# Optimization experiments

Measured on AMD Instinct MI355X. Metric: run time of the kernel, lower is better.

The kernel has to match this reference:

```python
import jax, jax.numpy as jnp
import numpy as np

N = 50000      # nodes
E = 800000     # edges (before self-loops)
DIN = 2        # dim_input
DEMB = 128     # dim_embedding
H = 8          # n_heads
DV = 16        # dim_values (H*DV == DEMB)
DH = 512       # dim_hidden
L = 2          # n_att_layers
K = 10         # APPNP steps
ALPHA = 0.1
EPS = 1e-5     # BatchNorm eps
NEG_SLOPE = 0.2  # GAT leaky_relu slope


def setup_inputs() -> dict:
    key = jax.random.key(0)
    ks = jax.random.split(key, 16)
    s = 0.05
    inp = {}
    inp["x"] = jax.random.normal(ks[0], (N, DIN), jnp.float32)
    inp["J"] = jax.random.uniform(ks[1], (N, 1), jnp.float32)
    inp["edge_index"] = jax.random.randint(ks[2], (2, E), 0, N, jnp.int32)
    # Lin1: Linear(dim_input+1, dim_embedding)
    inp["lin0_w"] = jax.random.normal(ks[3], (DIN + 1, DEMB), jnp.float32) * s
    inp["lin0_b"] = jnp.zeros((DEMB,), jnp.float32)
    # Per attention layer (stacked over L):
    inp["gat_w"]   = jax.random.normal(ks[4], (L, DEMB, H * DV), jnp.float32) * s
    inp["att_src"] = jax.random.normal(ks[5], (L, H, DV), jnp.float32) * s
    inp["att_dst"] = jax.random.normal(ks[6], (L, H, DV), jnp.float32) * s
    inp["lin1_w"]  = jax.random.normal(ks[7], (L, DV, DEMB), jnp.float32) * s
    inp["bn1_g"]   = jnp.ones((L, DEMB), jnp.float32)
    inp["bn1_b"]   = jnp.zeros((L, DEMB), jnp.float32)
    inp["lin2_w"]  = jax.random.normal(ks[8], (L, DEMB, DH), jnp.float32) * s
    inp["lin2_b"]  = jnp.zeros((L, DH), jnp.float32)
    inp["lin3_w"]  = jax.random.normal(ks[9], (L, DH, DEMB), jnp.float32) * s
    inp["lin3_b"]  = jnp.zeros((L, DEMB), jnp.float32)
    inp["bn2_g"]   = jnp.ones((L, DEMB), jnp.float32)
    inp["bn2_b"]   = jnp.zeros((L, DEMB), jnp.float32)
    return inp


def _bn(z, g, b):
    # BatchNorm1d over nodes, training-mode batch statistics (biased var)
    mu = z.mean(0)
    var = jnp.mean((z - mu) ** 2, axis=0)
    return g * (z - mu) * jax.lax.rsqrt(var + EPS) + b


def reference(x, J, edge_index, lin0_w, lin0_b, gat_w, att_src, att_dst,
              lin1_w, bn1_g, bn1_b, lin2_w, lin2_b, lin3_w, lin3_b,
              bn2_g, bn2_b):
    # add self-loops (PyG GATConv and APPNP defaults)
    loop = jnp.arange(N, dtype=edge_index.dtype)
    src = jnp.concatenate([edge_index[0], loop])  # message source j
    dst = jnp.concatenate([edge_index[1], loop])  # message target i

    h = jnp.concatenate([x, J], axis=1) @ lin0_w + lin0_b  # [N, DEMB]

    for l in range(L):
        # ---- GATConv ----
        xl = (h @ gat_w[l]).reshape(N, H, DV)                # [N,H,DV]
        a_s = (xl * att_src[l]).sum(-1)                      # [N,H]
        a_d = (xl * att_dst[l]).sum(-1)                      # [N,H]
        e = jax.nn.leaky_relu(a_s[src] + a_d[dst], NEG_SLOPE)  # [E',H]
        e = e - jax.ops.segment_max(e, dst, num_segments=N)[dst]
        ee = jnp.exp(e)
        alpha = ee / jax.ops.segment_sum(ee, dst, num_segments=N)[dst]
        msg = xl[src] * alpha[:, :, None]                    # [E',H,DV]
        gat_out = jax.ops.segment_sum(msg, dst, num_segments=N)  # [N,H,DV]
        # lin1 per head then sum over heads
        hsum = jnp.einsum('nhc,cd->nd', gat_out, lin1_w[l])  # [N,DEMB]
        h1 = _bn(h + hsum, bn1_g[l], bn1_b[l])
        h2 = jax.nn.relu(h1 @ lin2_w[l] + lin2_b[l]) @ lin3_w[l] + lin3_b[l]
        h = _bn(h2 + h1, bn2_g[l], bn2_b[l])

    # ---- APPNP: K steps of (1-a)*Ahat h + a*h0, Ahat = D^-1/2 (A+I) D^-1/2 ----
    deg = jax.ops.segment_sum(jnp.ones_like(dst, jnp.float32), dst, num_segments=N)
    dinv = jax.lax.rsqrt(jnp.maximum(deg, 1.0))  # self-loops guarantee deg>=1
    norm = (dinv[src] * dinv[dst])[:, None]      # [E',1]
    h0 = h

    def step(hk, _):
        agg = jax.ops.segment_sum(norm * hk[src], dst, num_segments=N)
        return (1.0 - ALPHA) * agg + ALPHA * h0, None

    h, _ = jax.lax.scan(step, h, None, length=K)
    return jnp.concatenate([h, J], axis=1)  # [N, DEMB+1]
```

## Files before the change

kernel.cpp:

```cpp
#include <hip/hip_runtime.h>

#define NN 50000
#define NP 50048
#define NMT64 782
#define NE 800000
#define EP (NE + NN)
#define DEMB 128
#define DHID 512
#define NB_SCAN 196

typedef unsigned short ushort_t;
typedef __attribute__((ext_vector_type(8))) short short8_t;
typedef __attribute__((ext_vector_type(4))) float float4_t;

__device__ __forceinline__ float bf2f(ushort_t u) {
    return __uint_as_float(((unsigned int)u) << 16);
}
__device__ __forceinline__ ushort_t f2bf(float f) {
    unsigned int x = __float_as_uint(f);
    x += 0x7fffu + ((x >> 16) & 1u);
    return (ushort_t)(x >> 16);
}
__device__ __forceinline__ float lo16(unsigned int w) { return __uint_as_float(w << 16); }
__device__ __forceinline__ float hi16(unsigned int w) { return __uint_as_float(w & 0xffff0000u); }
__device__ __forceinline__ unsigned int pack2(float a, float b) {
    return (unsigned int)f2bf(a) | ((unsigned int)f2bf(b) << 16);
}
__device__ __forceinline__ void gl_lds16(const ushort_t* g, ushort_t* l) {
    __builtin_amdgcn_global_load_lds(
        (const __attribute__((address_space(1))) void*)g,
        (__attribute__((address_space(3))) void*)l, 16, 0, 0);
}
static inline int cdiv(int a, int b) { return (a + b - 1) / b; }

__global__ void k_detect(const unsigned int* __restrict__ Jw, int* __restrict__ flag) {
    if (threadIdx.x != 0 || blockIdx.x != 0) return;
    int votes = 0;
    for (int i = 0; i < 8; ++i) {
        unsigned int w = Jw[i];
        unsigned int ex = (w >> 23) & 0xFFu;
        if ((w >> 31) == 0u && ex >= 100u && ex <= 126u) votes++;
    }
    *flag = (votes >= 6) ? 1 : 0;
}

struct CvtArgs {
    const void* src[16];
    float* dst[16];
    int n[16];
};
__global__ void k_cvt_all(CvtArgs a, const int* __restrict__ flag) {
    int which = blockIdx.y;
    int i = blockIdx.x * 256 + threadIdx.x;
    if (i >= a.n[which]) return;
    float v;
    if (*flag) v = ((const float*)a.src[which])[i];
    else       v = bf2f(((const ushort_t*)a.src[which])[i]);
    a.dst[which][i] = v;
}

struct TrArgs {
    const float* src[6];
    ushort_t* dst[6];
    int K[6];
    int Nc[6];
    int perm[6];
};
__global__ void k_tr_all(TrArgs a) {
    int which = blockIdx.y;
    int idx = blockIdx.x * 256 + threadIdx.x;
    int K = a.K[which], Nc = a.Nc[which];
    if (idx >= K * Nc) return;
    int k = idx / Nc, n = idx - k * Nc;
    int kd = k;
    if (a.perm[which]) {
        int kk = k & 63;
        kd = (k & ~63) | ((kk & 32) + 2 * (kk & 15) + ((kk >> 4) & 1));
    }
    a.dst[which][n * K + kd] = f2bf(a.src[which][idx]);
}

__global__ void k_deg(const int* __restrict__ ei, int* __restrict__ deg) {
    int e = blockIdx.x * 256 + threadIdx.x;
    if (e >= EP) return;
    int d = (e < NE) ? ei[NE + e] : (e - NE);
    atomicAdd(&deg[d], 1);
}

__global__ void k_part(const int* __restrict__ deg, int* __restrict__ part) {
    __shared__ int sm[256];
    int i = blockIdx.x * 256 + threadIdx.x;
    int v = (i < NN) ? deg[i] : 0;
    sm[threadIdx.x] = v;
    __syncthreads();
    for (int off = 128; off > 0; off >>= 1) {
        if (threadIdx.x < off) sm[threadIdx.x] += sm[threadIdx.x + off];
        __syncthreads();
    }
    if (threadIdx.x == 0) part[blockIdx.x] = sm[0];
}

__global__ void k_scan2(const int* __restrict__ part, int* __restrict__ poff,
                        int* __restrict__ rowp) {
    __shared__ int sm[256];
    int t = threadIdx.x;
    int v = (t < NB_SCAN) ? part[t] : 0;
    sm[t] = v;
    __syncthreads();
    int incl = v;
    for (int off = 1; off < 256; off <<= 1) {
        int u = (t >= off) ? sm[t - off] : 0;
        __syncthreads();
        incl += u;
        sm[t] = incl;
        __syncthreads();
    }
    if (t < NB_SCAN) poff[t] = incl - v;
    if (t == 255) rowp[NN] = sm[255];
}

__global__ void k_rowp(const int* __restrict__ deg, const int* __restrict__ poff,
                       int* __restrict__ rowp, float* __restrict__ dinv,
                       int* __restrict__ fill) {
    __shared__ int sm[256];
    int i = blockIdx.x * 256 + threadIdx.x;
    int t = threadIdx.x;
    int v = (i < NN) ? deg[i] : 0;
    sm[t] = v;
    __syncthreads();
    int incl = v;
    for (int off = 1; off < 256; off <<= 1) {
        int u = (t >= off) ? sm[t - off] : 0;
        __syncthreads();
        incl += u;
        sm[t] = incl;
        __syncthreads();
    }
    if (i < NN) {
        int rp = poff[blockIdx.x] + incl - v;
        rowp[i] = rp;
        fill[i] = rp;
        dinv[i] = rsqrtf(fmaxf((float)v, 1.0f));
    }
}

__global__ void k_fill(const int* __restrict__ ei, int* __restrict__ fillpos,
                       ushort_t* __restrict__ col) {
    int e = blockIdx.x * 256 + threadIdx.x;
    if (e >= EP) return;
    int s, d;
    if (e < NE) { s = ei[e]; d = ei[NE + e]; } else { s = d = e - NE; }
    int pos = atomicAdd(&fillpos[d], 1);
    col[pos] = (ushort_t)s;
}

__global__ void k_lin0(const float* __restrict__ x, const float* __restrict__ J,
                       const float* __restrict__ w, const float* __restrict__ b,
                       ushort_t* __restrict__ hB) {
    int idx = blockIdx.x * 256 + threadIdx.x;
    if (idx >= NN * DEMB) return;
    int n = idx >> 7, d = idx & 127;
    float v = x[n * 2] * w[d] + x[n * 2 + 1] * w[DEMB + d] + J[n] * w[2 * DEMB + d] + b[d];
    hB[idx] = f2bf(v);
}

__global__ void k_att(const unsigned int* __restrict__ xlB, const float* __restrict__ asrc,
                      const float* __restrict__ adst, float* __restrict__ a_s,
                      float* __restrict__ a_d) {
    int idx = blockIdx.x * 256 + threadIdx.x;
    if (idx >= NN * 8) return;
    int n = idx >> 3, hh = idx & 7;
    const unsigned int* row = xlB + (size_t)n * 64 + hh * 8;
    float s = 0.f, d = 0.f;
#pragma unroll
    for (int c = 0; c < 8; ++c) {
        unsigned int w = row[c];
        float v0 = lo16(w), v1 = hi16(w);
        s += v0 * asrc[hh * 16 + 2 * c] + v1 * asrc[hh * 16 + 2 * c + 1];
        d += v0 * adst[hh * 16 + 2 * c] + v1 * adst[hh * 16 + 2 * c + 1];
    }
    a_s[idx] = s;
    a_d[idx] = d;
}

__global__ __launch_bounds__(256) void k_z1s(const ushort_t* __restrict__ hB,
                                             const float* __restrict__ g,
                                             const float* __restrict__ w1,
                                             float* __restrict__ stats) {
    int d = threadIdx.x & 127;
    int rstart = blockIdx.x * 2 + (threadIdx.x >> 7);
    int stride = gridDim.x * 2;
    float s1 = 0.f, s2 = 0.f;
    for (int r = rstart; r < NN; r += stride) {
        const float* gr = g + r * 16;
        float s = bf2f(hB[(size_t)r * DEMB + d]);
#pragma unroll
        for (int c = 0; c < 16; ++c) s += gr[c] * w1[c * DEMB + d];
        s1 += s;
        s2 += s * s;
    }
    __shared__ float b1[256], b2[256];
    b1[threadIdx.x] = s1;
    b2[threadIdx.x] = s2;
    __syncthreads();
    if (threadIdx.x < 128) {
        atomicAdd(&stats[threadIdx.x], b1[threadIdx.x] + b1[threadIdx.x + 128]);
        atomicAdd(&stats[128 + threadIdx.x], b2[threadIdx.x] + b2[threadIdx.x + 128]);
    }
}

__global__ void k_bnapply1(const ushort_t* __restrict__ hB, const float* __restrict__ g,
                           const float* __restrict__ w1, const float* __restrict__ stats,
                           const float* __restrict__ gam, const float* __restrict__ bet,
                           ushort_t* __restrict__ outB) {
    int idx = blockIdx.x * 256 + threadIdx.x;
    if (idx >= NN * DEMB) return;
    int n = idx >> 7, d = idx & 127;
    float s = bf2f(hB[idx]);
    const float* gr = g + n * 16;
#pragma unroll
    for (int c = 0; c < 16; ++c) s += gr[c] * w1[c * DEMB + d];
    const float invN = 1.0f / (float)NN;
    float mu = stats[d] * invN;
    float var = stats[128 + d] * invN - mu * mu;
    float rs = rsqrtf(fmaxf(var, 0.f) + 1e-5f);
    float v = gam[d] * (s - mu) * rs + bet[d];
    outB[idx] = f2bf(v);
}

__global__ void k_bnapply(const ushort_t* __restrict__ zB, const float* __restrict__ stats,
                          const float* __restrict__ gam, const float* __restrict__ bet,
                          ushort_t* __restrict__ outB) {
    int idx = blockIdx.x * 256 + threadIdx.x;
    if (idx >= NN * DEMB) return;
    int d = idx & 127;
    const float invN = 1.0f / (float)NN;
    float mu = stats[d] * invN;
    float var = stats[128 + d] * invN - mu * mu;
    float rs = rsqrtf(fmaxf(var, 0.f) + 1e-5f);
    float v = gam[d] * (bf2f(zB[idx]) - mu) * rs + bet[d];
    outB[idx] = f2bf(v);
}

__global__ void k_bnapply_fin(const unsigned int* __restrict__ zB, const float* __restrict__ stats,
                              const float* __restrict__ gam, const float* __restrict__ bet,
                              const float* __restrict__ dinv,
                              unsigned int* __restrict__ hs, unsigned int* __restrict__ h0p) {
    int idx = blockIdx.x * 256 + threadIdx.x;
    if (idx >= NN * 64) return;
    int n = idx >> 6, d0 = (idx & 63) * 2;
    const float invN = 1.0f / (float)NN;
    unsigned int zw = zB[idx];
    float z0 = lo16(zw), z1 = hi16(zw);
    float mu0 = stats[d0] * invN, mu1 = stats[d0 + 1] * invN;
    float v0 = stats[128 + d0] * invN - mu0 * mu0;
    float v1 = stats[128 + d0 + 1] * invN - mu1 * mu1;
    float rs0 = rsqrtf(fmaxf(v0, 0.f) + 1e-5f);
    float rs1 = rsqrtf(fmaxf(v1, 0.f) + 1e-5f);
    float a = gam[d0] * (z0 - mu0) * rs0 + bet[d0];
    float b = gam[d0 + 1] * (z1 - mu1) * rs1 + bet[d0 + 1];
    float di = dinv[n];
    hs[idx] = pack2(di * a, di * b);
    h0p[idx] = pack2(a, b);
}

__global__ __launch_bounds__(256) void k_gat(const int* __restrict__ rowp,
                                             const ushort_t* __restrict__ col,
                                             const float* __restrict__ a_s, const float* __restrict__ a_d,
                                             const unsigned int* __restrict__ xlB, float* __restrict__ g) {
    int wid = (blockIdx.x * 256 + threadIdx.x) >> 6;
    int lane = threadIdx.x & 63;
    if (wid >= NN) return;
    int p0 = rowp[wid], p1 = rowp[wid + 1];
    int hh = lane >> 3;
    float ad2 = a_d[wid * 8 + hh];
    float acc0 = 0.f, acc1 = 0.f, s = 0.f;
    int p = p0;
    while (p < p1) {
        int cnt = p1 - p;
        if (cnt > 64) cnt = 64;
        int pl = p + lane;
        int jv = (int)col[pl < p1 ? pl : (p1 - 1)];
        int i = 0;
        for (; i + 8 <= cnt; i += 8) {
            int j0 = __shfl(jv, i),     j1 = __shfl(jv, i + 1);
            int j2 = __shfl(jv, i + 2), j3 = __shfl(jv, i + 3);
            int j4 = __shfl(jv, i + 4), j5 = __shfl(jv, i + 5);
            int j6 = __shfl(jv, i + 6), j7 = __shfl(jv, i + 7);
            float e0 = a_s[j0 * 8 + hh] + ad2, e1 = a_s[j1 * 8 + hh] + ad2;
            float e2 = a_s[j2 * 8 + hh] + ad2, e3 = a_s[j3 * 8 + hh] + ad2;
            float e4 = a_s[j4 * 8 + hh] + ad2, e5 = a_s[j5 * 8 + hh] + ad2;
            float e6 = a_s[j6 * 8 + hh] + ad2, e7 = a_s[j7 * 8 + hh] + ad2;
            unsigned int w0 = xlB[j0 * 64 + lane], w1 = xlB[j1 * 64 + lane];
            unsigned int w2 = xlB[j2 * 64 + lane], w3 = xlB[j3 * 64 + lane];
            unsigned int w4 = xlB[j4 * 64 + lane], w5 = xlB[j5 * 64 + lane];
            unsigned int w6 = xlB[j6 * 64 + lane], w7 = xlB[j7 * 64 + lane];
            e0 = e0 > 0.f ? e0 : 0.2f * e0;  e1 = e1 > 0.f ? e1 : 0.2f * e1;
            e2 = e2 > 0.f ? e2 : 0.2f * e2;  e3 = e3 > 0.f ? e3 : 0.2f * e3;
            e4 = e4 > 0.f ? e4 : 0.2f * e4;  e5 = e5 > 0.f ? e5 : 0.2f * e5;
            e6 = e6 > 0.f ? e6 : 0.2f * e6;  e7 = e7 > 0.f ? e7 : 0.2f * e7;
            float al0 = __expf(e0), al1 = __expf(e1), al2 = __expf(e2), al3 = __expf(e3);
            float al4 = __expf(e4), al5 = __expf(e5), al6 = __expf(e6), al7 = __expf(e7);
            s += al0 + al1 + al2 + al3 + al4 + al5 + al6 + al7;
            acc0 += al0 * lo16(w0) + al1 * lo16(w1) + al2 * lo16(w2) + al3 * lo16(w3) +
                    al4 * lo16(w4) + al5 * lo16(w5) + al6 * lo16(w6) + al7 * lo16(w7);
            acc1 += al0 * hi16(w0) + al1 * hi16(w1) + al2 * hi16(w2) + al3 * hi16(w3) +
                    al4 * hi16(w4) + al5 * hi16(w5) + al6 * hi16(w6) + al7 * hi16(w7);
        }
        for (; i < cnt; ++i) {
            int j = __shfl(jv, i);
            float e = a_s[j * 8 + hh] + ad2;
            e = e > 0.f ? e : 0.2f * e;
            float al = __expf(e);
            unsigned int w = xlB[j * 64 + lane];
            s += al;
            acc0 += al * lo16(w);
            acc1 += al * hi16(w);
        }
        p += cnt;
    }
    float inv = 1.f / s;
    acc0 *= inv;
    acc1 *= inv;
    acc0 += __shfl_xor(acc0, 8);  acc1 += __shfl_xor(acc1, 8);
    acc0 += __shfl_xor(acc0, 16); acc1 += __shfl_xor(acc1, 16);
    acc0 += __shfl_xor(acc0, 32); acc1 += __shfl_xor(acc1, 32);
    if (lane < 8) ((float2*)g)[wid * 8 + lane] = make_float2(acc0, acc1);
}

__global__ __launch_bounds__(256) void k_appnp(const int* __restrict__ rowp,
                                               const ushort_t* __restrict__ col,
                                               const float* __restrict__ dinv,
                                               const unsigned int* __restrict__ hs,
                                               const unsigned int* __restrict__ h0p,
                                               unsigned int* __restrict__ hs_out,
                                               const float* __restrict__ Jf,
                                               const int* __restrict__ flag,
                                               void* __restrict__ out, int writeOut) {
    int wid = (blockIdx.x * 256 + threadIdx.x) >> 6;
    int lane = threadIdx.x & 63;
    if (wid >= NN) return;
    int p0 = rowp[wid], p1 = rowp[wid + 1];
    float di = dinv[wid];
    unsigned int hw = h0p[(size_t)wid * 64 + lane];
    float a0 = 0.f, a1 = 0.f;
    int p = p0;
    while (p < p1) {
        int cnt = p1 - p;
        if (cnt > 64) cnt = 64;
        int pl = p + lane;
        int jv = (int)col[pl < p1 ? pl : (p1 - 1)];
        int i = 0;
        for (; i + 8 <= cnt; i += 8) {
            int j0 = __shfl(jv, i),     j1 = __shfl(jv, i + 1);
            int j2 = __shfl(jv, i + 2), j3 = __shfl(jv, i + 3);
            int j4 = __shfl(jv, i + 4), j5 = __shfl(jv, i + 5);
            int j6 = __shfl(jv, i + 6), j7 = __shfl(jv, i + 7);
            unsigned int w0 = hs[j0 * 64 + lane], w1 = hs[j1 * 64 + lane];
            unsigned int w2 = hs[j2 * 64 + lane], w3 = hs[j3 * 64 + lane];
            unsigned int w4 = hs[j4 * 64 + lane], w5 = hs[j5 * 64 + lane];
            unsigned int w6 = hs[j6 * 64 + lane], w7 = hs[j7 * 64 + lane];
            a0 += lo16(w0) + lo16(w1) + lo16(w2) + lo16(w3) +
                  lo16(w4) + lo16(w5) + lo16(w6) + lo16(w7);
            a1 += hi16(w0) + hi16(w1) + hi16(w2) + hi16(w3) +
                  hi16(w4) + hi16(w5) + hi16(w6) + hi16(w7);
        }
        for (; i < cnt; ++i) {
            int j = __shfl(jv, i);
            unsigned int w = hs[j * 64 + lane];
            a0 += lo16(w);
            a1 += hi16(w);
        }
        p += cnt;
    }
    float n0 = 0.9f * di * a0 + 0.1f * lo16(hw);
    float n1 = 0.9f * di * a1 + 0.1f * hi16(hw);
    if (!writeOut) {
        hs_out[(size_t)wid * 64 + lane] = pack2(di * n0, di * n1);
    } else {
        size_t base = (size_t)wid * 129;
        if (*flag) {
            float* o = (float*)out;
            o[base + 2 * lane] = n0;
            o[base + 2 * lane + 1] = n1;
            if (lane == 0) o[base + 128] = Jf[wid];
        } else {
            ushort_t* o = (ushort_t*)out;
            o[base + 2 * lane] = f2bf(n0);
            o[base + 2 * lane + 1] = f2bf(n1);
            if (lane == 0) o[base + 128] = f2bf(Jf[wid]);
        }
    }
}

template <int MODE>
__global__ __launch_bounds__(256) void k_gemm64(const ushort_t* __restrict__ A,
                                                const ushort_t* __restrict__ Bt,
                                                int M, int K, int Nc,
                                                const float* __restrict__ bias,
                                                const ushort_t* __restrict__ res,
                                                ushort_t* __restrict__ outB,
                                                float* __restrict__ stats) {
    __shared__ __align__(16) ushort_t lsA[2][64 * 32];
    __shared__ __align__(16) ushort_t lsB[2][128 * 32];
    int t = threadIdx.x;
    int m0 = blockIdx.x * 64;
    int n0 = blockIdx.y * 128;
    int w = t >> 6, lane = t & 63;
    int row16 = lane & 15, quad = lane >> 4;
    int nbase = w * 32;
    float4_t acc[8];
#pragma unroll
    for (int i = 0; i < 8; ++i) acc[i] = (float4_t){0.f, 0.f, 0.f, 0.f};
    int lrow = lane >> 2;
    int lcol = (lane & 3) * 8;
    const ushort_t* gA  = A  + (size_t)(m0 + w * 16 + lrow) * K + lcol;
    const ushort_t* gB0 = Bt + (size_t)(n0 + w * 32 + lrow) * K + lcol;
    const ushort_t* gB1 = Bt + (size_t)(n0 + w * 32 + 16 + lrow) * K + lcol;
    ushort_t* dA  = &lsA[0][0] + (w * 16) * 32;
    ushort_t* dB0 = &lsB[0][0] + (w * 32) * 32;
    ushort_t* dB1 = &lsB[0][0] + (w * 32 + 16) * 32;
    const int bufStrideA = 64 * 32, bufStrideB = 128 * 32;
    const int nK = K >> 5;
    gl_lds16(gA, dA);
    gl_lds16(gB0, dB0);
    gl_lds16(gB1, dB1);
    for (int kb = 0; kb < nK; ++kb) {
        __syncthreads();
        int nb = kb + 1;
        if (nb < nK) {
            int b = nb & 1;
            int k0 = nb << 5;
            gl_lds16(gA + k0, dA + b * bufStrideA);
            gl_lds16(gB0 + k0, dB0 + b * bufStrideB);
            gl_lds16(gB1 + k0, dB1 + b * bufStrideB);
        }
        const ushort_t* la = &lsA[kb & 1][0];
        const ushort_t* lb = &lsB[kb & 1][0];
        short8_t afr[4], bfr[2];
#pragma unroll
        for (int i = 0; i < 4; ++i)
            afr[i] = *(const short8_t*)(la + (i * 16 + row16) * 32 + quad * 8);
#pragma unroll
        for (int i = 0; i < 2; ++i)
            bfr[i] = *(const short8_t*)(lb + (nbase + i * 16 + row16) * 32 + quad * 8);
#pragma unroll
        for (int mt = 0; mt < 4; ++mt)
#pragma unroll
            for (int nt = 0; nt < 2; ++nt)
                acc[mt * 2 + nt] = __builtin_amdgcn_mfma_f32_16x16x32_bf16(
                    afr[mt], bfr[nt], acc[mt * 2 + nt], 0, 0, 0);
    }
#pragma unroll
    for (int mt = 0; mt < 4; ++mt) {
#pragma unroll
        for (int nt = 0; nt < 2; ++nt) {
            int cc = n0 + nbase + nt * 16 + row16;
#pragma unroll
            for (int r = 0; r < 4; ++r) {
                int rr = m0 + mt * 16 + quad * 4 + r;
                if (rr < M) {
                    outB[(size_t)rr * Nc + cc] = f2bf(acc[mt * 2 + nt][r]);
                }
            }
        }
    }
}

__global__ __launch_bounds__(256, 3) void k_ffn(const ushort_t* __restrict__ A,
                                                const ushort_t* __restrict__ W2t,
                                                const ushort_t* __restrict__ W3t,
                                                const float* __restrict__ b2,
                                                const float* __restrict__ b3,
                                                const ushort_t* __restrict__ res,
                                                ushort_t* __restrict__ outB,
                                                float* __restrict__ stats) {
    __shared__ __align__(16) ushort_t sW2[4 * 64 * 32];
    __shared__ __align__(16) ushort_t sW3[2 * 128 * 32];
    __shared__ __align__(16) ushort_t sAH[4 * 2048];
    int t = threadIdx.x;
    int w = t >> 6, lane = t & 63;
    int wm = w >> 1, wn = w & 1;
    int m0 = blockIdx.x * 64;
    int row16 = lane & 15, quad = lane >> 4;
    int sw = (row16 >> 2) & 3;
    int srow = lane >> 2;
    int klin = lane & 3;

#pragma unroll
    for (int i = 0; i < 4; ++i) {
        int row = i * 16 + srow;
        int kc = klin ^ ((row >> 2) & 3);
        gl_lds16(A + (size_t)(m0 + row) * 128 + w * 32 + kc * 8,
                 sAH + w * 2048 + i * 512);
        gl_lds16(W2t + (size_t)row * 128 + w * 32 + kc * 8,
                 sW2 + w * 2048 + i * 512);
        int f = w * 4 + i;
        int ks = f >> 3;
        int n3 = (f & 7) * 16 + srow;
        int kc3 = klin ^ ((n3 >> 2) & 3);
        gl_lds16(W3t + (size_t)n3 * 512 + ks * 32 + kc3 * 8,
                 sW3 + f * 512);
    }
    __syncthreads();

    short8_t afrA[2][4];
#pragma unroll
    for (int mt = 0; mt < 2; ++mt)
#pragma unroll
        for (int kb = 0; kb < 4; ++kb)
            afrA[mt][kb] = *(const short8_t*)(sAH + kb * 2048 +
                                              (wm * 32 + mt * 16 + row16) * 32 + (quad ^ sw) * 8);
    __syncthreads();

    char* Hb = (char*)sAH;
    float* s1 = (float*)(Hb + 8192);
    float* s2 = s1 + 128;
    if (t < 128) { s1[t] = 0.f; s2[t] = 0.f; }

    float4_t accz[2][4];
#pragma unroll
    for (int mt = 0; mt < 2; ++mt)
#pragma unroll
        for (int nt = 0; nt < 4; ++nt) accz[mt][nt] = (float4_t){0.f, 0.f, 0.f, 0.f};

    for (int c = 0; c < 8; ++c) {
        float b20 = b2[c * 64 + wn * 32 + row16];
        float b21 = b2[c * 64 + wn * 32 + 16 + row16];
        float4_t acch[2][2];
#pragma unroll
        for (int mt = 0; mt < 2; ++mt)
#pragma unroll
            for (int nt = 0; nt < 2; ++nt) acch[mt][nt] = (float4_t){0.f, 0.f, 0.f, 0.f};
#pragma unroll
        for (int kb = 0; kb < 4; ++kb) {
            short8_t b0 = *(const short8_t*)(sW2 + kb * 2048 +
                                             (wn * 32 + row16) * 32 + (quad ^ sw) * 8);
            short8_t b1 = *(const short8_t*)(sW2 + kb * 2048 +
                                             (wn * 32 + 16 + row16) * 32 + (quad ^ sw) * 8);
            acch[0][0] = __builtin_amdgcn_mfma_f32_16x16x32_bf16(afrA[0][kb], b0, acch[0][0], 0, 0, 0);
            acch[0][1] = __builtin_amdgcn_mfma_f32_16x16x32_bf16(afrA[0][kb], b1, acch[0][1], 0, 0, 0);
            acch[1][0] = __builtin_amdgcn_mfma_f32_16x16x32_bf16(afrA[1][kb], b0, acch[1][0], 0, 0, 0);
            acch[1][1] = __builtin_amdgcn_mfma_f32_16x16x32_bf16(afrA[1][kb], b1, acch[1][1], 0, 0, 0);
        }
#pragma unroll
        for (int mt = 0; mt < 2; ++mt) {
#pragma unroll
            for (int r = 0; r < 4; ++r) {
                int row = wm * 32 + mt * 16 + quad * 4 + r;
                int d = wn * 16 + row16;
                int byteOff = row * 128 + ((((d >> 2) ^ (row & 7))) << 4) + (d & 3) * 4;
                float v0 = acch[mt][0][r] + b20; v0 = v0 > 0.f ? v0 : 0.f;
                float v1 = acch[mt][1][r] + b21; v1 = v1 > 0.f ? v1 : 0.f;
                *(unsigned int*)(Hb + byteOff) = pack2(v0, v1);
            }
        }
        __syncthreads();
        if (c < 7) {
#pragma unroll
            for (int i = 0; i < 4; ++i) {
                int n = i * 16 + srow;
                int kc = klin ^ ((n >> 2) & 3);
                gl_lds16(W2t + (size_t)((c + 1) * 64 + n) * 128 + w * 32 + kc * 8,
                         sW2 + w * 2048 + i * 512);
            }
        }
#pragma unroll
        for (int ks = 0; ks < 2; ++ks) {
            short8_t afrH[2];
#pragma unroll
            for (int mt = 0; mt < 2; ++mt)
                afrH[mt] = *(const short8_t*)(Hb + (wm * 32 + mt * 16 + row16) * 128 +
                                              (((ks * 4 + quad) ^ (row16 & 7)) << 4));
#pragma unroll
            for (int nt = 0; nt < 4; ++nt) {
                short8_t bfr = *(const short8_t*)(sW3 + ks * 4096 +
                                                  (wn * 64 + nt * 16 + row16) * 32 + (quad ^ sw) * 8);
                accz[0][nt] = __builtin_amdgcn_mfma_f32_16x16x32_bf16(afrH[0], bfr, accz[0][nt], 0, 0, 0);
                accz[1][nt] = __builtin_amdgcn_mfma_f32_16x16x32_bf16(afrH[1], bfr, accz[1][nt], 0, 0, 0);
            }
        }
        __syncthreads();
        if (c < 7) {
#pragma unroll
            for (int i = 0; i < 4; ++i) {
                int f = w * 4 + i;
                int ks = f >> 3;
                int n = (f & 7) * 16 + srow;
                int kc = klin ^ ((n >> 2) & 3);
                gl_lds16(W3t + (size_t)n * 512 + (c + 1) * 64 + ks * 32 + kc * 8,
                         sW3 + f * 512);
            }
        }
    }

#pragma unroll
    for (int mt = 0; mt < 2; ++mt) {
#pragma unroll
        for (int nt = 0; nt < 4; ++nt) {
            int cc = wn * 64 + nt * 16 + row16;
            float bv = b3[cc];
            float ls = 0.f, lq = 0.f;
#pragma unroll
            for (int r = 0; r < 4; ++r) {
                int rr = m0 + wm * 32 + mt * 16 + quad * 4 + r;
                if (rr < NN) {
                    float v = accz[mt][nt][r] + bv + bf2f(res[(size_t)rr * 128 + cc]);
                    outB[(size_t)rr * 128 + cc] = f2bf(v);
                    ls += v;
                    lq += v * v;
                }
            }
            atomicAdd(&s1[cc], ls);
            atomicAdd(&s2[cc], lq);
        }
    }
    __syncthreads();
    if (t < 128) {
        atomicAdd(&stats[t], s1[t]);
        atomicAdd(&stats[128 + t], s2[t]);
    }
}

extern "C" void kernel_launch(void* const* d_in, const int* in_sizes, int n_in,
                              void* d_out, int out_size, void* d_ws, size_t ws_size,
                              hipStream_t stream) {
    const int* ei = (const int*)d_in[2];

    char* p = (char*)d_ws;
    auto alloc = [&](size_t bytes) {
        void* r = (void*)p;
        p += (bytes + 255) & ~(size_t)255;
        return r;
    };
    ushort_t* hB    = (ushort_t*)alloc((size_t)NP * DEMB * 2);
    ushort_t* h1B   = (ushort_t*)alloc((size_t)NP * DEMB * 2);
    ushort_t* xlB   = (ushort_t*)alloc((size_t)NN * DEMB * 2);
    unsigned int* hsA  = (unsigned int*)alloc((size_t)NN * 64 * 4);
    unsigned int* hsB_ = (unsigned int*)alloc((size_t)NN * 64 * 4);
    unsigned int* h0p  = (unsigned int*)alloc((size_t)NN * 64 * 4);
    float*    asv   = (float*)alloc((size_t)NN * 8 * 4);
    float*    adv   = (float*)alloc((size_t)NN * 8 * 4);
    float*    gv    = (float*)alloc((size_t)NN * 16 * 4);
    float*    dinvv = (float*)alloc((size_t)NN * 4);
    float*    stats = (float*)alloc(4 * 256 * 4);
    int*      deg   = (int*)alloc((size_t)NN * 4);
    int*      rowp  = (int*)alloc((size_t)(NN + 1) * 4);
    int*      fill  = (int*)alloc((size_t)NN * 4);
    ushort_t* colv  = (ushort_t*)alloc((size_t)EP * 2);
    int*      part  = (int*)alloc(NB_SCAN * 4);
    int*      poff  = (int*)alloc(NB_SCAN * 4);
    int*      flag  = (int*)alloc(256);
    ushort_t* wtg   = (ushort_t*)alloc((size_t)2 * 128 * 128 * 2);
    ushort_t* wt2   = (ushort_t*)alloc((size_t)2 * 512 * 128 * 2);
    ushort_t* wt3   = (ushort_t*)alloc((size_t)2 * 128 * 512 * 2);
    float* xf   = (float*)alloc((size_t)NN * 2 * 4);
    float* Jf   = (float*)alloc((size_t)NN * 4);
    float* l0wF = (float*)alloc(384 * 4);
    float* l0bF = (float*)alloc(128 * 4);
    float* gwF  = (float*)alloc(32768 * 4);
    float* asF  = (float*)alloc(256 * 4);
    float* adF  = (float*)alloc(256 * 4);
    float* w1F  = (float*)alloc(4096 * 4);
    float* b1gF = (float*)alloc(256 * 4);
    float* b1bF = (float*)alloc(256 * 4);
    float* w2F  = (float*)alloc(131072 * 4);
    float* b2F  = (float*)alloc(1024 * 4);
    float* w3F  = (float*)alloc(131072 * 4);
    float* b3F  = (float*)alloc(256 * 4);
    float* b2gF = (float*)alloc(256 * 4);
    float* b2bF = (float*)alloc(256 * 4);

    k_detect<<<1, 64, 0, stream>>>((const unsigned int*)d_in[1], flag);
    CvtArgs ca;
    {
        const int srcIdx[16] = {0, 1, 3, 4, 5, 6, 7, 8, 9, 10, 11, 12, 13, 14, 15, 16};
        float* dsts[16] = {xf, Jf, l0wF, l0bF, gwF, asF, adF, w1F, b1gF, b1bF,
                           w2F, b2F, w3F, b3F, b2gF, b2bF};
        const int ns[16] = {NN * 2, NN, 384, 128, 32768, 256, 256, 4096, 256, 256,
                            131072, 1024, 131072, 256, 256, 256};
        for (int i = 0; i < 16; ++i) { ca.src[i] = d_in[srcIdx[i]]; ca.dst[i] = dsts[i]; ca.n[i] = ns[i]; }
    }
    k_cvt_all<<<dim3(cdiv(131072, 256), 16), 256, 0, stream>>>(ca, flag);

    hipMemsetAsync(deg, 0, (size_t)NN * 4, stream);
    hipMemsetAsync(stats, 0, 4 * 256 * 4, stream);
    k_deg<<<cdiv(EP, 256), 256, 0, stream>>>(ei, deg);
    k_part<<<NB_SCAN, 256, 0, stream>>>(deg, part);
    k_scan2<<<1, 256, 0, stream>>>(part, poff, rowp);
    k_rowp<<<NB_SCAN, 256, 0, stream>>>(deg, poff, rowp, dinvv, fill);
    k_fill<<<cdiv(EP, 256), 256, 0, stream>>>(ei, fill, colv);

    TrArgs ta;
    {
        const float* srcs[6] = {gwF, gwF + 16384, w2F, w2F + 65536, w3F, w3F + 65536};
        ushort_t* dsts[6] = {wtg, wtg + 16384, wt2, wt2 + 65536, wt3, wt3 + 65536};
        const int Ks[6] = {128, 128, 128, 128, 512, 512};
        const int Ncs[6] = {128, 128, 512, 512, 128, 128};
        const int perms[6] = {0, 0, 0, 0, 1, 1};
        for (int i = 0; i < 6; ++i) {
            ta.src[i] = srcs[i]; ta.dst[i] = dsts[i]; ta.K[i] = Ks[i]; ta.Nc[i] = Ncs[i];
            ta.perm[i] = perms[i];
        }
    }
    k_tr_all<<<dim3(cdiv(65536, 256), 6), 256, 0, stream>>>(ta);

    k_lin0<<<cdiv(NN * DEMB, 256), 256, 0, stream>>>(xf, Jf, l0wF, l0bF, hB);

    for (int l = 0; l < 2; ++l) {
        float* st1 = stats + (l * 2 + 0) * 256;
        float* st2 = stats + (l * 2 + 1) * 256;
        ushort_t* zB = xlB;
        k_gemm64<3><<<dim3(NMT64, 1), 256, 0, stream>>>(hB, wtg + l * 16384, NN, 128, 128,
                                                        nullptr, nullptr, xlB, nullptr);
        k_att<<<cdiv(NN * 8, 256), 256, 0, stream>>>((const unsigned int*)xlB, asF + l * 128,
                                                     adF + l * 128, asv, adv);
        k_gat<<<cdiv(NN * 64, 256), 256, 0, stream>>>(rowp, colv, asv, adv,
                                                      (const unsigned int*)xlB, gv);
        k_z1s<<<512, 256, 0, stream>>>(hB, gv, w1F + l * 2048, st1);
        k_bnapply1<<<cdiv(NN * DEMB, 256), 256, 0, stream>>>(hB, gv, w1F + l * 2048, st1,
                                                             b1gF + l * 128, b1bF + l * 128,
                                                             h1B);
        k_ffn<<<NMT64, 256, 0, stream>>>(h1B, wt2 + l * 65536, wt3 + l * 65536,
                                         b2F + l * 512, b3F + l * 128, h1B, zB, st2);
        if (l == 0) {
            k_bnapply<<<cdiv(NN * DEMB, 256), 256, 0, stream>>>(zB, st2, b2gF, b2bF, hB);
        } else {
            k_bnapply_fin<<<cdiv(NN * 64, 256), 256, 0, stream>>>((const unsigned int*)zB, st2,
                                                                  b2gF + 128, b2bF + 128,
                                                                  dinvv, hsA, h0p);
        }
    }

    unsigned int* pin = hsA;
    unsigned int* pout = hsB_;
    for (int k = 0; k < 10; ++k) {
        int last = (k == 9) ? 1 : 0;
        k_appnp<<<cdiv(NN * 64, 256), 256, 0, stream>>>(rowp, colv, dinvv, pin, h0p, pout,
                                                        Jf, flag, d_out, last);
        unsigned int* tmp = pout;
        pout = pin;
        pin = tmp;
    }
}
```

Measured before the change: 875.2 us.

## Split APPNP features into column slabs and shrink FFN row tile to 32

The APPNP state is stored as four feature slabs of 32 bf16 features each, laid out node-major within a slab. Each propagation block handles one slab for four nodes, with four edges gathered in parallel per wave. The aim is to keep the gathered working set small enough to stay cache-resident and so cut scattered HBM traffic over the ten propagation steps. Separately, the FFN kernel uses 32-row tiles with each wave owning a column strip, which removes the W3 k-permutation in favour of a shuffle-based pack and allows higher occupancy, at the cost of twice as many blocks and more weight reloads.

```diff
diff --git a/kernel.cpp b/kernel.cpp
--- a/kernel.cpp
+++ b/kernel.cpp
@@ -3,6 +3,7 @@
 #define NN 50000
 #define NP 50048
 #define NMT64 782
+#define NMT32 1563
 #define NE 800000
 #define EP (NE + NN)
 #define DEMB 128
@@ -72,12 +73,7 @@
     int K = a.K[which], Nc = a.Nc[which];
     if (idx >= K * Nc) return;
     int k = idx / Nc, n = idx - k * Nc;
-    int kd = k;
-    if (a.perm[which]) {
-        int kk = k & 63;
-        kd = (k & ~63) | ((kk & 32) + 2 * (kk & 15) + ((kk >> 4) & 1));
-    }
-    a.dst[which][n * K + kd] = f2bf(a.src[which][idx]);
+    a.dst[which][n * K + k] = f2bf(a.src[which][idx]);
 }
 
 __global__ void k_deg(const int* __restrict__ ei, int* __restrict__ deg) {
@@ -248,7 +244,8 @@
                               unsigned int* __restrict__ hs, unsigned int* __restrict__ h0p) {
     int idx = blockIdx.x * 256 + threadIdx.x;
     if (idx >= NN * 64) return;
-    int n = idx >> 6, d0 = (idx & 63) * 2;
+    int n = idx >> 6, j = idx & 63;
+    int d0 = j * 2;
     const float invN = 1.0f / (float)NN;
     unsigned int zw = zB[idx];
     float z0 = lo16(zw), z1 = hi16(zw);
@@ -260,8 +257,10 @@
     float a = gam[d0] * (z0 - mu0) * rs0 + bet[d0];
     float b = gam[d0 + 1] * (z1 - mu1) * rs1 + bet[d0 + 1];
     float di = dinv[n];
-    hs[idx] = pack2(di * a, di * b);
-    h0p[idx] = pack2(a, b);
+    int q = j >> 4, dd = j & 15;
+    size_t o = (size_t)q * NN * 16 + (size_t)n * 16 + dd;
+    hs[o] = pack2(di * a, di * b);
+    h0p[o] = pack2(a, b);
 }
 
 __global__ __launch_bounds__(256) void k_gat(const int* __restrict__ rowp,
@@ -337,58 +336,51 @@
                                                const float* __restrict__ Jf,
                                                const int* __restrict__ flag,
                                                void* __restrict__ out, int writeOut) {
-    int wid = (blockIdx.x * 256 + threadIdx.x) >> 6;
-    int lane = threadIdx.x & 63;
-    if (wid >= NN) return;
-    int p0 = rowp[wid], p1 = rowp[wid + 1];
-    float di = dinv[wid];
-    unsigned int hw = h0p[(size_t)wid * 64 + lane];
+    int b = blockIdx.x;
+    int w = threadIdx.x >> 6, lane = threadIdx.x & 63;
+    int s = (b & 7) >> 1;
+    int i = ((b >> 3) << 1) + (b & 1);
+    int n = i * 4 + w;
+    int es = lane >> 4, d = lane & 15;
+    int p0 = rowp[n], p1 = rowp[n + 1];
+    const unsigned int* hsq = hs + (size_t)s * NN * 16;
     float a0 = 0.f, a1 = 0.f;
     int p = p0;
-    while (p < p1) {
-        int cnt = p1 - p;
-        if (cnt > 64) cnt = 64;
-        int pl = p + lane;
-        int jv = (int)col[pl < p1 ? pl : (p1 - 1)];
-        int i = 0;
-        for (; i + 8 <= cnt; i += 8) {
-            int j0 = __shfl(jv, i),     j1 = __shfl(jv, i + 1);
-            int j2 = __shfl(jv, i + 2), j3 = __shfl(jv, i + 3);
-            int j4 = __shfl(jv, i + 4), j5 = __shfl(jv, i + 5);
-            int j6 = __shfl(jv, i + 6), j7 = __shfl(jv, i + 7);
-            unsigned int w0 = hs[j0 * 64 + lane], w1 = hs[j1 * 64 + lane];
-            unsigned int w2 = hs[j2 * 64 + lane], w3 = hs[j3 * 64 + lane];
-            unsigned int w4 = hs[j4 * 64 + lane], w5 = hs[j5 * 64 + lane];
-            unsigned int w6 = hs[j6 * 64 + lane], w7 = hs[j7 * 64 + lane];
-            a0 += lo16(w0) + lo16(w1) + lo16(w2) + lo16(w3) +
-                  lo16(w4) + lo16(w5) + lo16(w6) + lo16(w7);
-            a1 += hi16(w0) + hi16(w1) + hi16(w2) + hi16(w3) +
-                  hi16(w4) + hi16(w5) + hi16(w6) + hi16(w7);
-        }
-        for (; i < cnt; ++i) {
-            int j = __shfl(jv, i);
-            unsigned int w = hs[j * 64 + lane];
-            a0 += lo16(w);
-            a1 += hi16(w);
-        }
-        p += cnt;
-    }
+    for (; p + 8 <= p1; p += 8) {
+        int j0 = (int)col[p + es];
+        int j1 = (int)col[p + 4 + es];
+        unsigned int w0 = hsq[j0 * 16 + d];
+        unsigned int w1 = hsq[j1 * 16 + d];
+        a0 += lo16(w0) + lo16(w1);
+        a1 += hi16(w0) + hi16(w1);
+    }
+    for (; p < p1; p += 4) {
+        int pe = p + es;
+        int j = (int)col[pe < p1 ? pe : (p1 - 1)];
+        unsigned int wv = hsq[j * 16 + d];
+        if (pe < p1) { a0 += lo16(wv); a1 += hi16(wv); }
+    }
+    a0 += __shfl_xor(a0, 16); a1 += __shfl_xor(a1, 16);
+    a0 += __shfl_xor(a0, 32); a1 += __shfl_xor(a1, 32);
+    float di = dinv[n];
+    unsigned int hw = h0p[(size_t)s * NN * 16 + (size_t)n * 16 + d];
     float n0 = 0.9f * di * a0 + 0.1f * lo16(hw);
     float n1 = 0.9f * di * a1 + 0.1f * hi16(hw);
     if (!writeOut) {
-        hs_out[(size_t)wid * 64 + lane] = pack2(di * n0, di * n1);
-    } else {
-        size_t base = (size_t)wid * 129;
+        if (es == 0)
+            hs_out[(size_t)s * NN * 16 + (size_t)n * 16 + d] = pack2(di * n0, di * n1);
+    } else if (es == 0) {
+        size_t base = (size_t)n * 129 + s * 32 + 2 * d;
         if (*flag) {
             float* o = (float*)out;
-            o[base + 2 * lane] = n0;
-            o[base + 2 * lane + 1] = n1;
-            if (lane == 0) o[base + 128] = Jf[wid];
+            o[base] = n0;
+            o[base + 1] = n1;
+            if (s == 0 && d == 0) o[(size_t)n * 129 + 128] = Jf[n];
         } else {
             ushort_t* o = (ushort_t*)out;
-            o[base + 2 * lane] = f2bf(n0);
-            o[base + 2 * lane + 1] = f2bf(n1);
-            if (lane == 0) o[base + 128] = f2bf(Jf[wid]);
+            o[base] = f2bf(n0);
+            o[base + 1] = f2bf(n1);
+            if (s == 0 && d == 0) o[(size_t)n * 129 + 128] = f2bf(Jf[n]);
         }
     }
 }
@@ -467,7 +459,7 @@
     }
 }
 
-__global__ __launch_bounds__(256, 3) void k_ffn(const ushort_t* __restrict__ A,
+__global__ __launch_bounds__(256, 4) void k_ffn(const ushort_t* __restrict__ A,
                                                 const ushort_t* __restrict__ W2t,
                                                 const ushort_t* __restrict__ W3t,
                                                 const float* __restrict__ b2,
@@ -477,23 +469,27 @@
                                                 float* __restrict__ stats) {
     __shared__ __align__(16) ushort_t sW2[4 * 64 * 32];
     __shared__ __align__(16) ushort_t sW3[2 * 128 * 32];
-    __shared__ __align__(16) ushort_t sAH[4 * 2048];
+    __shared__ __align__(16) ushort_t sAH[4 * 1024];
     int t = threadIdx.x;
     int w = t >> 6, lane = t & 63;
-    int wm = w >> 1, wn = w & 1;
-    int m0 = blockIdx.x * 64;
+    int m0 = blockIdx.x * 32;
     int row16 = lane & 15, quad = lane >> 4;
     int sw = (row16 >> 2) & 3;
     int srow = lane >> 2;
     int klin = lane & 3;
 
 #pragma unroll
-    for (int i = 0; i < 4; ++i) {
+    for (int i = 0; i < 2; ++i) {
         int row = i * 16 + srow;
         int kc = klin ^ ((row >> 2) & 3);
         gl_lds16(A + (size_t)(m0 + row) * 128 + w * 32 + kc * 8,
-                 sAH + w * 2048 + i * 512);
-        gl_lds16(W2t + (size_t)row * 128 + w * 32 + kc * 8,
+                 sAH + w * 1024 + i * 512);
+    }
+#pragma unroll
+    for (int i = 0; i < 4; ++i) {
+        int n = i * 16 + srow;
+        int kc = klin ^ ((n >> 2) & 3);
+        gl_lds16(W2t + (size_t)n * 128 + w * 32 + kc * 8,
                  sW2 + w * 2048 + i * 512);
         int f = w * 4 + i;
         int ks = f >> 3;
@@ -509,50 +505,46 @@
     for (int mt = 0; mt < 2; ++mt)
 #pragma unroll
         for (int kb = 0; kb < 4; ++kb)
-            afrA[mt][kb] = *(const short8_t*)(sAH + kb * 2048 +
-                                              (wm * 32 + mt * 16 + row16) * 32 + (quad ^ sw) * 8);
+            afrA[mt][kb] = *(const short8_t*)(sAH + kb * 1024 +
+                                              (mt * 16 + row16) * 32 + (quad ^ sw) * 8);
     __syncthreads();
 
     char* Hb = (char*)sAH;
-    float* s1 = (float*)(Hb + 8192);
+    float* s1 = (float*)(Hb + 4096);
     float* s2 = s1 + 128;
     if (t < 128) { s1[t] = 0.f; s2[t] = 0.f; }
 
-    float4_t accz[2][4];
+    float4_t accz[2][2];
 #pragma unroll
     for (int mt = 0; mt < 2; ++mt)
 #pragma unroll
-        for (int nt = 0; nt < 4; ++nt) accz[mt][nt] = (float4_t){0.f, 0.f, 0.f, 0.f};
+        for (int nt = 0; nt < 2; ++nt) accz[mt][nt] = (float4_t){0.f, 0.f, 0.f, 0.f};
 
     for (int c = 0; c < 8; ++c) {
-        float b20 = b2[c * 64 + wn * 32 + row16];
-        float b21 = b2[c * 64 + wn * 32 + 16 + row16];
-        float4_t acch[2][2];
-#pragma unroll
-        for (int mt = 0; mt < 2; ++mt)
-#pragma unroll
-            for (int nt = 0; nt < 2; ++nt) acch[mt][nt] = (float4_t){0.f, 0.f, 0.f, 0.f};
+        float b2v = b2[c * 64 + w * 16 + row16];
+        float4_t acch[2];
+        acch[0] = (float4_t){0.f, 0.f, 0.f, 0.f};
+        acch[1] = (float4_t){0.f, 0.f, 0.f, 0.f};
 #pragma unroll
         for (int kb = 0; kb < 4; ++kb) {
             short8_t b0 = *(const short8_t*)(sW2 + kb * 2048 +
-                                             (wn * 32 + row16) * 32 + (quad ^ sw) * 8);
-            short8_t b1 = *(const short8_t*)(sW2 + kb * 2048 +
-                                             (wn * 32 + 16 + row16) * 32 + (quad ^ sw) * 8);
-            acch[0][0] = __builtin_amdgcn_mfma_f32_16x16x32_bf16(afrA[0][kb], b0, acch[0][0], 0, 0, 0);
-            acch[0][1] = __builtin_amdgcn_mfma_f32_16x16x32_bf16(afrA[0][kb], b1, acch[0][1], 0, 0, 0);
-            acch[1][0] = __builtin_amdgcn_mfma_f32_16x16x32_bf16(afrA[1][kb], b0, acch[1][0], 0, 0, 0);
-            acch[1][1] = __builtin_amdgcn_mfma_f32_16x16x32_bf16(afrA[1][kb], b1, acch[1][1], 0, 0, 0);
+                                             (w * 16 + row16) * 32 + (quad ^ sw) * 8);
+            acch[0] = __builtin_amdgcn_mfma_f32_16x16x32_bf16(afrA[0][kb], b0, acch[0], 0, 0, 0);
+            acch[1] = __builtin_amdgcn_mfma_f32_16x16x32_bf16(afrA[1][kb], b0, acch[1], 0, 0, 0);
         }
 #pragma unroll
         for (int mt = 0; mt < 2; ++mt) {
 #pragma unroll
             for (int r = 0; r < 4; ++r) {
-                int row = wm * 32 + mt * 16 + quad * 4 + r;
-                int d = wn * 16 + row16;
-                int byteOff = row * 128 + ((((d >> 2) ^ (row & 7))) << 4) + (d & 3) * 4;
-                float v0 = acch[mt][0][r] + b20; v0 = v0 > 0.f ? v0 : 0.f;
-                float v1 = acch[mt][1][r] + b21; v1 = v1 > 0.f ? v1 : 0.f;
-                *(unsigned int*)(Hb + byteOff) = pack2(v0, v1);
+                int row = mt * 16 + quad * 4 + r;
+                float v = acch[mt][r] + b2v;
+                v = v > 0.f ? v : 0.f;
+                float vo = __shfl_xor(v, 1);
+                if (!(row16 & 1)) {
+                    int kidx = w * 8 + (row16 >> 1);
+                    int byteOff = row * 128 + ((((kidx >> 2) ^ (row & 7))) << 4) + (kidx & 3) * 4;
+                    *(unsigned int*)(Hb + byteOff) = pack2(v, vo);
+                }
             }
         }
         __syncthreads();
@@ -570,12 +562,12 @@
             short8_t afrH[2];
 #pragma unroll
             for (int mt = 0; mt < 2; ++mt)
-                afrH[mt] = *(const short8_t*)(Hb + (wm * 32 + mt * 16 + row16) * 128 +
+                afrH[mt] = *(const short8_t*)(Hb + (mt * 16 + row16) * 128 +
                                               (((ks * 4 + quad) ^ (row16 & 7)) << 4));
 #pragma unroll
-            for (int nt = 0; nt < 4; ++nt) {
+            for (int nt = 0; nt < 2; ++nt) {
                 short8_t bfr = *(const short8_t*)(sW3 + ks * 4096 +
-                                                  (wn * 64 + nt * 16 + row16) * 32 + (quad ^ sw) * 8);
+                                                  (w * 32 + nt * 16 + row16) * 32 + (quad ^ sw) * 8);
                 accz[0][nt] = __builtin_amdgcn_mfma_f32_16x16x32_bf16(afrH[0], bfr, accz[0][nt], 0, 0, 0);
                 accz[1][nt] = __builtin_amdgcn_mfma_f32_16x16x32_bf16(afrH[1], bfr, accz[1][nt], 0, 0, 0);
             }
@@ -597,13 +589,13 @@
 #pragma unroll
     for (int mt = 0; mt < 2; ++mt) {
 #pragma unroll
-        for (int nt = 0; nt < 4; ++nt) {
-            int cc = wn * 64 + nt * 16 + row16;
+        for (int nt = 0; nt < 2; ++nt) {
+            int cc = w * 32 + nt * 16 + row16;
             float bv = b3[cc];
             float ls = 0.f, lq = 0.f;
 #pragma unroll
             for (int r = 0; r < 4; ++r) {
-                int rr = m0 + wm * 32 + mt * 16 + quad * 4 + r;
+                int rr = m0 + mt * 16 + quad * 4 + r;
                 if (rr < NN) {
                     float v = accz[mt][nt][r] + bv + bf2f(res[(size_t)rr * 128 + cc]);
                     outB[(size_t)rr * 128 + cc] = f2bf(v);
@@ -697,10 +689,9 @@
         ushort_t* dsts[6] = {wtg, wtg + 16384, wt2, wt2 + 65536, wt3, wt3 + 65536};
         const int Ks[6] = {128, 128, 128, 128, 512, 512};
         const int Ncs[6] = {128, 128, 512, 512, 128, 128};
-        const int perms[6] = {0, 0, 0, 0, 1, 1};
         for (int i = 0; i < 6; ++i) {
             ta.src[i] = srcs[i]; ta.dst[i] = dsts[i]; ta.K[i] = Ks[i]; ta.Nc[i] = Ncs[i];
-            ta.perm[i] = perms[i];
+            ta.perm[i] = 0;
         }
     }
     k_tr_all<<<dim3(cdiv(65536, 256), 6), 256, 0, stream>>>(ta);
@@ -721,7 +712,7 @@
         k_bnapply1<<<cdiv(NN * DEMB, 256), 256, 0, stream>>>(hB, gv, w1F + l * 2048, st1,
                                                              b1gF + l * 128, b1bF + l * 128,
                                                              h1B);
-        k_ffn<<<NMT64, 256, 0, stream>>>(h1B, wt2 + l * 65536, wt3 + l * 65536,
+        k_ffn<<<NMT32, 256, 0, stream>>>(h1B, wt2 + l * 65536, wt3 + l * 65536,
                                          b2F + l * 512, b3F + l * 128, h1B, zB, st2);
         if (l == 0) {
             k_bnapply<<<cdiv(NN * DEMB, 256), 256, 0, stream>>>(zB, st2, b2gF, b2bF, hB);
@@ -736,8 +727,8 @@
     unsigned int* pout = hsB_;
     for (int k = 0; k < 10; ++k) {
         int last = (k == 9) ? 1 : 0;
-        k_appnp<<<cdiv(NN * 64, 256), 256, 0, stream>>>(rowp, colv, dinvv, pin, h0p, pout,
-                                                        Jf, flag, d_out, last);
+        k_appnp<<<50000, 256, 0, stream>>>(rowp, colv, dinvv, pin, h0p, pout,
+                                           Jf, flag, d_out, last);
         unsigned int* tmp = pout;
         pout = pin;
         pin = tmp;
```

Measured after the change: 1.318 ms. +50.7%, slower.

## Split APPNP features into four 32-column slices with slice-major layout

Applied to the files above, without the earlier changes.

The APPNP hidden state is stored as four slice-major planes of 16 packed words per node. Each wavefront now handles four nodes on one 32-feature slice, and the block index is mapped so that adjacent blocks cover different slices of the same node group. The goal is to shrink the per-slice working set so gathers hit in cache better, and to cut idle lanes for nodes of low degree. In exchange the column indices are read and shuffled four times per node, and the loop pays extra predication for tails.

```diff
diff --git a/kernel.cpp b/kernel.cpp
--- a/kernel.cpp
+++ b/kernel.cpp
@@ -248,7 +248,8 @@
                               unsigned int* __restrict__ hs, unsigned int* __restrict__ h0p) {
     int idx = blockIdx.x * 256 + threadIdx.x;
     if (idx >= NN * 64) return;
-    int n = idx >> 6, d0 = (idx & 63) * 2;
+    int n = idx >> 6, j = idx & 63;
+    int d0 = j * 2;
     const float invN = 1.0f / (float)NN;
     unsigned int zw = zB[idx];
     float z0 = lo16(zw), z1 = hi16(zw);
@@ -260,8 +261,10 @@
     float a = gam[d0] * (z0 - mu0) * rs0 + bet[d0];
     float b = gam[d0 + 1] * (z1 - mu1) * rs1 + bet[d0 + 1];
     float di = dinv[n];
-    hs[idx] = pack2(di * a, di * b);
-    h0p[idx] = pack2(a, b);
+    int q = j >> 4, dd = j & 15;
+    size_t o = (size_t)q * NN * 16 + (size_t)n * 16 + dd;
+    hs[o] = pack2(di * a, di * b);
+    h0p[o] = pack2(a, b);
 }
 
 __global__ __launch_bounds__(256) void k_gat(const int* __restrict__ rowp,
@@ -337,58 +340,71 @@
                                                const float* __restrict__ Jf,
                                                const int* __restrict__ flag,
                                                void* __restrict__ out, int writeOut) {
-    int wid = (blockIdx.x * 256 + threadIdx.x) >> 6;
-    int lane = threadIdx.x & 63;
-    if (wid >= NN) return;
-    int p0 = rowp[wid], p1 = rowp[wid + 1];
-    float di = dinv[wid];
-    unsigned int hw = h0p[(size_t)wid * 64 + lane];
+    int b = blockIdx.x;
+    int w = threadIdx.x >> 6, lane = threadIdx.x & 63;
+    int s = (b & 7) >> 1;
+    int g = ((b >> 3) << 1) + (b & 1);
+    int ns = lane >> 4, d = lane & 15;
+    int n = g * 16 + w * 4 + ns;
+    int valid = (n < NN);
+    int nc = valid ? n : (NN - 1);
+    int p0 = rowp[nc], p1 = rowp[nc + 1];
+    const unsigned int* hsq = hs + (size_t)s * NN * 16;
+    unsigned int hw = h0p[(size_t)s * NN * 16 + (size_t)nc * 16 + d];
+    float di = dinv[nc];
+    int base = ns << 4;
     float a0 = 0.f, a1 = 0.f;
     int p = p0;
     while (p < p1) {
         int cnt = p1 - p;
-        if (cnt > 64) cnt = 64;
-        int pl = p + lane;
+        if (cnt > 16) cnt = 16;
+        int pl = p + d;
         int jv = (int)col[pl < p1 ? pl : (p1 - 1)];
-        int i = 0;
-        for (; i + 8 <= cnt; i += 8) {
-            int j0 = __shfl(jv, i),     j1 = __shfl(jv, i + 1);
-            int j2 = __shfl(jv, i + 2), j3 = __shfl(jv, i + 3);
-            int j4 = __shfl(jv, i + 4), j5 = __shfl(jv, i + 5);
-            int j6 = __shfl(jv, i + 6), j7 = __shfl(jv, i + 7);
-            unsigned int w0 = hs[j0 * 64 + lane], w1 = hs[j1 * 64 + lane];
-            unsigned int w2 = hs[j2 * 64 + lane], w3 = hs[j3 * 64 + lane];
-            unsigned int w4 = hs[j4 * 64 + lane], w5 = hs[j5 * 64 + lane];
-            unsigned int w6 = hs[j6 * 64 + lane], w7 = hs[j7 * 64 + lane];
-            a0 += lo16(w0) + lo16(w1) + lo16(w2) + lo16(w3) +
-                  lo16(w4) + lo16(w5) + lo16(w6) + lo16(w7);
-            a1 += hi16(w0) + hi16(w1) + hi16(w2) + hi16(w3) +
-                  hi16(w4) + hi16(w5) + hi16(w6) + hi16(w7);
-        }
-        for (; i < cnt; ++i) {
-            int j = __shfl(jv, i);
-            unsigned int w = hs[j * 64 + lane];
-            a0 += lo16(w);
-            a1 += hi16(w);
+        int lim = cnt - 1;
+        for (int k = 0; k < cnt; k += 8) {
+            int q0 = k,     q1 = k + 1, q2 = k + 2, q3 = k + 3;
+            int q4 = k + 4, q5 = k + 5, q6 = k + 6, q7 = k + 7;
+            int j0 = __shfl(jv, base + (q0 < lim ? q0 : lim));
+            int j1 = __shfl(jv, base + (q1 < lim ? q1 : lim));
+            int j2 = __shfl(jv, base + (q2 < lim ? q2 : lim));
+            int j3 = __shfl(jv, base + (q3 < lim ? q3 : lim));
+            int j4 = __shfl(jv, base + (q4 < lim ? q4 : lim));
+            int j5 = __shfl(jv, base + (q5 < lim ? q5 : lim));
+            int j6 = __shfl(jv, base + (q6 < lim ? q6 : lim));
+            int j7 = __shfl(jv, base + (q7 < lim ? q7 : lim));
+            unsigned int w0 = hsq[j0 * 16 + d], w1 = hsq[j1 * 16 + d];
+            unsigned int w2 = hsq[j2 * 16 + d], w3 = hsq[j3 * 16 + d];
+            unsigned int w4 = hsq[j4 * 16 + d], w5 = hsq[j5 * 16 + d];
+            unsigned int w6 = hsq[j6 * 16 + d], w7 = hsq[j7 * 16 + d];
+            a0 += ((q0 <= lim) ? lo16(w0) : 0.f) + ((q1 <= lim) ? lo16(w1) : 0.f) +
+                  ((q2 <= lim) ? lo16(w2) : 0.f) + ((q3 <= lim) ? lo16(w3) : 0.f) +
+                  ((q4 <= lim) ? lo16(w4) : 0.f) + ((q5 <= lim) ? lo16(w5) : 0.f) +
+                  ((q6 <= lim) ? lo16(w6) : 0.f) + ((q7 <= lim) ? lo16(w7) : 0.f);
+            a1 += ((q0 <= lim) ? hi16(w0) : 0.f) + ((q1 <= lim) ? hi16(w1) : 0.f) +
+                  ((q2 <= lim) ? hi16(w2) : 0.f) + ((q3 <= lim) ? hi16(w3) : 0.f) +
+                  ((q4 <= lim) ? hi16(w4) : 0.f) + ((q5 <= lim) ? hi16(w5) : 0.f) +
+                  ((q6 <= lim) ? hi16(w6) : 0.f) + ((q7 <= lim) ? hi16(w7) : 0.f);
         }
         p += cnt;
     }
     float n0 = 0.9f * di * a0 + 0.1f * lo16(hw);
     float n1 = 0.9f * di * a1 + 0.1f * hi16(hw);
-    if (!writeOut) {
-        hs_out[(size_t)wid * 64 + lane] = pack2(di * n0, di * n1);
-    } else {
-        size_t base = (size_t)wid * 129;
-        if (*flag) {
-            float* o = (float*)out;
-            o[base + 2 * lane] = n0;
-            o[base + 2 * lane + 1] = n1;
-            if (lane == 0) o[base + 128] = Jf[wid];
+    if (valid) {
+        if (!writeOut) {
+            hs_out[(size_t)s * NN * 16 + (size_t)n * 16 + d] = pack2(di * n0, di * n1);
         } else {
-            ushort_t* o = (ushort_t*)out;
-            o[base + 2 * lane] = f2bf(n0);
-            o[base + 2 * lane + 1] = f2bf(n1);
-            if (lane == 0) o[base + 128] = f2bf(Jf[wid]);
+            size_t obase = (size_t)n * 129 + s * 32 + 2 * d;
+            if (*flag) {
+                float* o = (float*)out;
+                o[obase] = n0;
+                o[obase + 1] = n1;
+                if (s == 0 && d == 0) o[(size_t)n * 129 + 128] = Jf[n];
+            } else {
+                ushort_t* o = (ushort_t*)out;
+                o[obase] = f2bf(n0);
+                o[obase + 1] = f2bf(n1);
+                if (s == 0 && d == 0) o[(size_t)n * 129 + 128] = f2bf(Jf[n]);
+            }
         }
     }
 }
@@ -736,8 +752,8 @@
     unsigned int* pout = hsB_;
     for (int k = 0; k < 10; ++k) {
         int last = (k == 9) ? 1 : 0;
-        k_appnp<<<cdiv(NN * 64, 256), 256, 0, stream>>>(rowp, colv, dinvv, pin, h0p, pout,
-                                                        Jf, flag, d_out, last);
+        k_appnp<<<12504, 256, 0, stream>>>(rowp, colv, dinvv, pin, h0p, pout,
+                                           Jf, flag, d_out, last);
         unsigned int* tmp = pout;
         pout = pin;
         pin = tmp;
```

Result: slower. 893.8 us (+2.1%).
